# Kernel optimization log

Hardware: AMD Instinct MI355X
Metric: run time of the kernel (lower is better)

The kernel has to match this reference:

```python
import jax, jax.numpy as jnp
import numpy as np

INPUT_SIZE = 1024
HIDDEN_SIZE = 1024
BATCH = 8192


def setup_inputs() -> dict:
    key = jax.random.key(0)
    ks = jax.random.split(key, 10)
    H, I, B = HIDDEN_SIZE, INPUT_SIZE, BATCH
    s = 1.0 / np.sqrt(H)  # scale params so activations stay in sane range
    return {
        "input": jax.random.normal(ks[0], (B, I), jnp.float32),
        "hx": jax.random.normal(ks[1], (B, H), jnp.float32),
        "cx": jax.random.normal(ks[2], (B, H), jnp.float32),
        "att": jax.random.normal(ks[3], (B, I), jnp.float32),
        "weight_ih": jax.random.normal(ks[4], (4 * H, I), jnp.float32) * s,
        "weight_hh": jax.random.normal(ks[5], (4 * H, H), jnp.float32) * s,
        "bias_ih": jax.random.normal(ks[6], (4 * H,), jnp.float32),
        "bias_hh": jax.random.normal(ks[7], (4 * H,), jnp.float32),
        "weight_att": jax.random.normal(ks[8], (2 * H, I), jnp.float32) * s,
        "bias_att": jax.random.normal(ks[9], (2 * H,), jnp.float32),
    }


def reference(input, hx, cx, att, weight_ih, weight_hh, bias_ih, bias_hh,
              weight_att, bias_att):
    H = weight_hh.shape[1]
    # gates: [B, 4H]
    gates = input @ weight_ih.T + bias_ih + hx @ weight_hh.T + bias_hh
    att_gates = att @ weight_att.T + bias_att  # [B, 2H]
    ingate, forgetgate, cellgate, outgate = jnp.split(gates, 4, axis=1)
    ingate_att, attgate = jnp.split(att_gates, 2, axis=1)
    ingate = jax.nn.sigmoid(ingate)
    forgetgate = jax.nn.sigmoid(forgetgate)
    cellgate = jnp.tanh(cellgate)
    ingate_att = jax.nn.sigmoid(ingate_att)
    attgate = jnp.tanh(attgate)
    outgate = jax.nn.sigmoid(outgate)
    cy = forgetgate * cx + ingate * cellgate + ingate_att * attgate
    hy = outgate * jnp.tanh(cy)
    return (hy, cy)
```

## Files before the change

kernel.cpp:

```cpp
#include <hip/hip_runtime.h>


typedef __attribute__((ext_vector_type(8))) __bf16 bf16x8;
typedef __attribute__((ext_vector_type(8))) unsigned short ushort8;
typedef __attribute__((ext_vector_type(4))) float f32x4;

#define AS1 __attribute__((address_space(1)))
#define AS3 __attribute__((address_space(3)))

__device__ __forceinline__ void gld16(const unsigned short* g, unsigned short* l) {
    __builtin_amdgcn_global_load_lds((const AS1 void*)g, (AS3 void*)l, 16, 0, 0);
}

__device__ __forceinline__ unsigned short f2bf(float f) {
    unsigned int u = __builtin_bit_cast(unsigned int, f);
    u += 0x7fffu + ((u >> 16) & 1u);
    return (unsigned short)(u >> 16);
}

__device__ __forceinline__ float sigmoidf_(float x) { return 1.f / (1.f + __expf(-x)); }
__device__ __forceinline__ float tanhf_(float x) {
    float e = __expf(-2.f * fabsf(x));
    float t = (1.f - e) / (1.f + e);
    return x >= 0.f ? t : -t;
}

__device__ __forceinline__ bf16x8 ldfrag(const unsigned short* p) {
    return __builtin_bit_cast(bf16x8, *(const ushort8*)p);
}

#define BARRIER __builtin_amdgcn_s_barrier()
#define LGKM0   asm volatile("s_waitcnt lgkmcnt(0)" ::: "memory")
#define VMW_(n) asm volatile("s_waitcnt vmcnt(" #n ")" ::: "memory")
#define VMW(n)  VMW_(n)
#define PRIO1   __builtin_amdgcn_s_setprio(1)
#define PRIO0   __builtin_amdgcn_s_setprio(0)
#define MFMA16(a, b, c) __builtin_amdgcn_mfma_f32_16x16x32_bf16(a, b, c, 0, 0, 0)

__global__ void cast_all_k(const float* __restrict__ input, const float* __restrict__ hx,
                           const float* __restrict__ att,   const float* __restrict__ w_ih,
                           const float* __restrict__ w_hh,  const float* __restrict__ w_att,
                           const float* __restrict__ b_ih,  const float* __restrict__ b_hh,
                           unsigned short* __restrict__ XH, unsigned short* __restrict__ ATTb,
                           unsigned short* __restrict__ W4, unsigned short* __restrict__ WA,
                           float* __restrict__ bias4)
{
    int gid = blockIdx.x * blockDim.x + threadIdx.x;
    if (gid < 4096) bias4[gid] = b_ih[gid] + b_hh[gid];
    const int total = 4456448;
    for (int i = gid; i < total; i += gridDim.x * blockDim.x) {
        const float* src; unsigned short* dst; int ld, off, rel;
        if (i < 1048576)      { src = input; dst = XH;   ld = 2048; off = 0;    rel = i; }
        else if (i < 2097152) { src = hx;    dst = XH;   ld = 2048; off = 1024; rel = i - 1048576; }
        else if (i < 3145728) { src = att;   dst = ATTb; ld = 1024; off = 0;    rel = i - 2097152; }
        else if (i < 3670016) { src = w_ih;  dst = W4;   ld = 2048; off = 0;    rel = i - 3145728; }
        else if (i < 4194304) { src = w_hh;  dst = W4;   ld = 2048; off = 1024; rel = i - 3670016; }
        else                  { src = w_att; dst = WA;   ld = 1024; off = 0;    rel = i - 4194304; }
        int e = rel * 8;
        int r = e >> 10, c = e & 1023;
        const float4 v0 = *(const float4*)(src + e);
        const float4 v1 = *(const float4*)(src + e + 4);
        ushort8 p;
        p[0] = f2bf(v0.x); p[1] = f2bf(v0.y); p[2] = f2bf(v0.z); p[3] = f2bf(v0.w);
        p[4] = f2bf(v1.x); p[5] = f2bf(v1.y); p[6] = f2bf(v1.z); p[7] = f2bf(v1.w);
        *(ushort8*)(dst + r * ld + off + c) = p;
    }
}

__global__ __launch_bounds__(512, 2) void fused_gemm_k(
    const unsigned short* __restrict__ XH, const unsigned short* __restrict__ W4,
    const unsigned short* __restrict__ ATTb, const unsigned short* __restrict__ WA,
    const float* __restrict__ bias4, const float* __restrict__ bias_att,
    const float* __restrict__ cx, float* __restrict__ out)
{
    __shared__ unsigned short As[2][16384];
    __shared__ unsigned short Bs[2][16384];

    const int tid  = threadIdx.x;
    const int wave = tid >> 6, lane = tid & 63;
    const int l15 = lane & 15, quad = lane >> 4;
    const int wr = wave >> 2, wn = wave & 3;

    const int orig = blockIdx.x;
    const int k    = orig >> 3, xcd = orig & 7;
    const int row0 = (k >> 1) * 256;
    const int n0   = (xcd * 2 + (k & 1)) * 64;

    const int rl = tid >> 3;
    const int c8 = (tid & 7) ^ (rl & 7);
    unsigned aG = (unsigned)(row0 + rl) * 2048u + (unsigned)c8 * 8u;
    unsigned bG = (unsigned)(((rl >> 4) & 3) * 1024 + n0 + (rl & 15)) * 2048u + (unsigned)c8 * 8u;
    unsigned aA = (unsigned)(row0 + rl) * 1024u + (unsigned)c8 * 8u;
    unsigned bA = (unsigned)(((rl >> 4) & 1) * 1024 + n0 + ((rl >> 5) & 1) * 16 + (rl & 15)) * 1024u
                  + (unsigned)c8 * 8u;

    auto stageA_att = [&](int buf) {
#pragma unroll
        for (int h = 0; h < 2; ++h)
#pragma unroll
            for (int p = 0; p < 2; ++p)
                gld16(ATTb + aA + (unsigned)(h * 131072 + p * 65536),
                      &As[buf][h * 8192 + (tid + p * 512) * 8]);
        aA += 64;
    };
    auto stageB_att = [&](int buf) {
#pragma unroll
        for (int h = 0; h < 2; ++h)
            gld16(WA + bA + (unsigned)(h * 32768), &Bs[buf][(h * 512 + tid) * 8]);
        bA += 64;
    };
    auto stageA_g = [&](int buf) {
#pragma unroll
        for (int h = 0; h < 2; ++h)
#pragma unroll
            for (int p = 0; p < 2; ++p)
                gld16(XH + aG + (unsigned)(h * 262144 + p * 131072),
                      &As[buf][h * 8192 + (tid + p * 512) * 8]);
        aG += 64;
    };
    auto stageB_g = [&](int buf) {
#pragma unroll
        for (int h = 0; h < 2; ++h)
#pragma unroll
            for (int p = 0; p < 2; ++p)
                gld16(W4 + bG + (unsigned)(h * 65536 + p * 32768),
                      &Bs[buf][h * 8192 + (tid + p * 512) * 8]);
        bG += 64;
    };

    const int swz0 = (quad ^ (l15 & 7)) * 8;
    const int swz1 = ((4 + quad) ^ (l15 & 7)) * 8;
    const int aro  = (wr * 128 + l15) * 64;
    const int brG  = (wn * 64 + l15) * 64;
    const int brA  = (wn * 32 + l15) * 64;

    const f32x4 z = {0.f, 0.f, 0.f, 0.f};

    f32x4 acc2[8][2];
#pragma unroll
    for (int i = 0; i < 8; ++i) { acc2[i][0] = z; acc2[i][1] = z; }

    auto att_slice = [&](int buf, int sw) {
        bf16x8 aS[8], bS[2];
#pragma unroll
        for (int i = 0; i < 8; ++i) aS[i] = ldfrag(&As[buf][aro + i * 1024 + sw]);
#pragma unroll
        for (int j = 0; j < 2; ++j) bS[j] = ldfrag(&Bs[buf][brA + j * 1024 + sw]);
        BARRIER; LGKM0;
        PRIO1;
#pragma unroll
        for (int i = 0; i < 8; ++i)
#pragma unroll
            for (int j = 0; j < 2; ++j)
                acc2[i][j] = MFMA16(aS[i], bS[j], acc2[i][j]);
        PRIO0;
        BARRIER;
    };

    stageA_att(0); stageB_att(0);
    for (int g = 0; g < 8; ++g) {
        stageA_att(1); stageB_att(1);
        VMW(6); BARRIER;
        att_slice(0, swz0);
        att_slice(0, swz1);
        if (g < 7) { stageA_att(0); stageB_att(0); VMW(6); }
        else       { VMW(0); }
        BARRIER;
        att_slice(1, swz0);
        att_slice(1, swz1);
    }

    const int col = n0 + wn * 16 + l15;
    f32x4 attp[8];
    {
        const float ba0 = bias_att[col], ba1 = bias_att[1024 + col];
#pragma unroll
        for (int i = 0; i < 8; ++i)
#pragma unroll
            for (int r = 0; r < 4; ++r)
                attp[i][r] = sigmoidf_(acc2[i][0][r] + ba0) * tanhf_(acc2[i][1][r] + ba1);
    }

    f32x4 acc[8][4];
#pragma unroll
    for (int i = 0; i < 8; ++i)
#pragma unroll
        for (int j = 0; j < 4; ++j) acc[i][j] = z;

    auto gates_group = [&](int buf, bool iss) {
        bf16x8 aF[4], aH0[4], aH1[4], bS0[4], bS1[4];
#pragma unroll
        for (int i = 0; i < 4; ++i) aF[i] = ldfrag(&As[buf][aro + i * 1024 + swz0]);
#pragma unroll
        for (int j = 0; j < 4; ++j) bS0[j] = ldfrag(&Bs[buf][brG + j * 1024 + swz0]);
        BARRIER; LGKM0;
        PRIO1;
#pragma unroll
        for (int i = 0; i < 4; ++i)
#pragma unroll
            for (int j = 0; j < 4; ++j)
                acc[i][j] = MFMA16(aF[i], bS0[j], acc[i][j]);
        PRIO0;
        BARRIER;
#pragma unroll
        for (int i = 0; i < 4; ++i) aF[i] = ldfrag(&As[buf][aro + i * 1024 + swz1]);
#pragma unroll
        for (int j = 0; j < 4; ++j) bS1[j] = ldfrag(&Bs[buf][brG + j * 1024 + swz1]);
        BARRIER; LGKM0;
        PRIO1;
#pragma unroll
        for (int i = 0; i < 4; ++i)
#pragma unroll
            for (int j = 0; j < 4; ++j)
                acc[i][j] = MFMA16(aF[i], bS1[j], acc[i][j]);
        PRIO0;
        BARRIER;
#pragma unroll
        for (int i = 0; i < 4; ++i) {
            aH0[i] = ldfrag(&As[buf][aro + (4 + i) * 1024 + swz0]);
            aH1[i] = ldfrag(&As[buf][aro + (4 + i) * 1024 + swz1]);
        }
        if (iss) stageB_g(buf);
        BARRIER; LGKM0;
        PRIO1;
#pragma unroll
        for (int i = 0; i < 4; ++i)
#pragma unroll
            for (int j = 0; j < 4; ++j)
                acc[4 + i][j] = MFMA16(aH0[i], bS0[j], acc[4 + i][j]);
        PRIO0;
        BARRIER;
        if (iss) stageA_g(buf);
        PRIO1;
#pragma unroll
        for (int i = 0; i < 4; ++i)
#pragma unroll
            for (int j = 0; j < 4; ++j)
                acc[4 + i][j] = MFMA16(aH1[i], bS1[j], acc[4 + i][j]);
        PRIO0;
    };

    stageA_g(0); stageB_g(0); stageA_g(1); stageB_g(1);
    VMW(8); BARRIER;
#pragma unroll 2
    for (int t = 0; t < 30; ++t) {
        gates_group(t & 1, true);
        VMW(8); BARRIER;
    }
    gates_group(0, false); VMW(0); BARRIER;
    gates_group(1, false);

    float* sF = (float*)(&As[0][0]);
    float* sC = (float*)(&Bs[0][0]);
    const float bi  = bias4[col];
    const float bff = bias4[1024 + col];
    const float bg  = bias4[2048 + col];
    const float bo  = bias4[3072 + col];
    const int lcol  = wn * 16 + l15;
    const int CYOFF = 8192 * 1024;

#pragma unroll
    for (int i = 0; i < 8; ++i)
#pragma unroll
        for (int r = 0; r < 4; ++r) {
            const int lr = wr * 128 + i * 16 + quad * 4 + r;
            const int pc = lcol ^ (((lr >> 2) & 1) << 4);
            sF[lr * 64 + pc] = sigmoidf_(acc[i][1][r] + bff);
            sC[lr * 64 + pc] = sigmoidf_(acc[i][0][r] + bi) * tanhf_(acc[i][2][r] + bg)
                               + attp[i][r];
        }
    BARRIER;

    const int rr = tid >> 4;
    const int cc = (tid & 15) * 4;
#pragma unroll
    for (int p = 0; p < 8; ++p) {
        const int row = p * 32 + rr;
        const int pcc = cc ^ (((row >> 2) & 1) << 4);
        f32x4 fg4 = *(f32x4*)&sF[row * 64 + pcc];
        f32x4 cp4 = *(f32x4*)&sC[row * 64 + pcc];
        const float4 cx4 = *(const float4*)&cx[(row0 + row) * 1024 + n0 + cc];
        f32x4 cy4;
        cy4[0] = fg4[0] * cx4.x + cp4[0];
        cy4[1] = fg4[1] * cx4.y + cp4[1];
        cy4[2] = fg4[2] * cx4.z + cp4[2];
        cy4[3] = fg4[3] * cx4.w + cp4[3];
        *(f32x4*)&out[CYOFF + (row0 + row) * 1024 + n0 + cc] = cy4;
        *(f32x4*)&sF[row * 64 + pcc] = cy4;
    }
    BARRIER;

#pragma unroll
    for (int i = 0; i < 8; ++i)
#pragma unroll
        for (int r = 0; r < 4; ++r) {
            const int lr = wr * 128 + i * 16 + quad * 4 + r;
            const int pc = lcol ^ (((lr >> 2) & 1) << 4);
            sC[lr * 64 + pc] = sigmoidf_(acc[i][3][r] + bo);
        }
    BARRIER;

#pragma unroll
    for (int p = 0; p < 8; ++p) {
        const int row = p * 32 + rr;
        const int pcc = cc ^ (((row >> 2) & 1) << 4);
        f32x4 og4 = *(f32x4*)&sC[row * 64 + pcc];
        f32x4 cy4 = *(f32x4*)&sF[row * 64 + pcc];
        f32x4 hy4;
        hy4[0] = og4[0] * tanhf_(cy4[0]);
        hy4[1] = og4[1] * tanhf_(cy4[1]);
        hy4[2] = og4[2] * tanhf_(cy4[2]);
        hy4[3] = og4[3] * tanhf_(cy4[3]);
        *(f32x4*)&out[(row0 + row) * 1024 + n0 + cc] = hy4;
    }
}

extern "C" void kernel_launch(void* const* d_in, const int* in_sizes, int n_in,
                              void* d_out, int out_size, void* d_ws, size_t ws_size,
                              hipStream_t stream) {
    const float* input = (const float*)d_in[0];
    const float* hx    = (const float*)d_in[1];
    const float* cx    = (const float*)d_in[2];
    const float* att   = (const float*)d_in[3];
    const float* w_ih  = (const float*)d_in[4];
    const float* w_hh  = (const float*)d_in[5];
    const float* b_ih  = (const float*)d_in[6];
    const float* b_hh  = (const float*)d_in[7];
    const float* w_att = (const float*)d_in[8];
    const float* b_att = (const float*)d_in[9];
    float* out = (float*)d_out;

    char* ws = (char*)d_ws;
    unsigned short* XH   = (unsigned short*)(ws);
    unsigned short* ATTb = (unsigned short*)(ws + 33554432);
    unsigned short* W4   = (unsigned short*)(ws + 50331648);
    unsigned short* WA   = (unsigned short*)(ws + 67108864);
    float* bias4         = (float*)(ws + 71303168);

    cast_all_k<<<8704, 256, 0, stream>>>(input, hx, att, w_ih, w_hh, w_att,
                                         b_ih, b_hh, XH, ATTb, W4, WA, bias4);
    fused_gemm_k<<<512, 512, 0, stream>>>(XH, W4, ATTb, WA, bias4, b_att, cx, out);
}
```

Measured before the change: 403.4 us.

## Remap block-to-XCD tiling and reorder MFMA sub-tile schedule in gates loop

Changes the block index mapping so each XCD handles a contiguous set of row tiles across all column tiles, instead of a fixed set of column tiles. The intent is to improve L2 reuse of the activation rows within an XCD. The gates inner loop is also restructured to load both K-halves of the A fragments up front and to split B into low and high column pairs. This reorders the MFMA phases, interleaves LDS loads with compute differently, and raises register use for fragments. An extra barrier is added before the epilogue reuses shared memory.

```diff
diff --git a/kernel.cpp b/kernel.cpp
--- a/kernel.cpp
+++ b/kernel.cpp
@@ -81,10 +81,10 @@
     const int l15 = lane & 15, quad = lane >> 4;
     const int wr = wave >> 2, wn = wave & 3;
 
-    const int orig = blockIdx.x;
-    const int k    = orig >> 3, xcd = orig & 7;
-    const int row0 = (k >> 1) * 256;
-    const int n0   = (xcd * 2 + (k & 1)) * 64;
+    const int orig  = blockIdx.x;
+    const int xcd   = orig & 7, local = orig >> 3;
+    const int row0  = (xcd * 4 + (local & 3)) * 256;
+    const int n0    = (local >> 2) * 64;
 
     const int rl = tid >> 3;
     const int c8 = (tid & 7) ^ (rl & 7);
@@ -188,31 +188,42 @@
         for (int j = 0; j < 4; ++j) acc[i][j] = z;
 
     auto gates_group = [&](int buf, bool iss) {
-        bf16x8 aF[4], aH0[4], aH1[4], bS0[4], bS1[4];
-#pragma unroll
-        for (int i = 0; i < 4; ++i) aF[i] = ldfrag(&As[buf][aro + i * 1024 + swz0]);
-#pragma unroll
-        for (int j = 0; j < 4; ++j) bS0[j] = ldfrag(&Bs[buf][brG + j * 1024 + swz0]);
+        bf16x8 aF0[4], aF1[4], aH0[4], aH1[4], bL0[2], bL1[2], bH0[2], bH1[2];
+#pragma unroll
+        for (int i = 0; i < 4; ++i) {
+            aF0[i] = ldfrag(&As[buf][aro + i * 1024 + swz0]);
+            aF1[i] = ldfrag(&As[buf][aro + i * 1024 + swz1]);
+        }
+#pragma unroll
+        for (int j = 0; j < 2; ++j) {
+            bL0[j] = ldfrag(&Bs[buf][brG + j * 1024 + swz0]);
+            bL1[j] = ldfrag(&Bs[buf][brG + j * 1024 + swz1]);
+        }
         BARRIER; LGKM0;
         PRIO1;
 #pragma unroll
         for (int i = 0; i < 4; ++i)
 #pragma unroll
-            for (int j = 0; j < 4; ++j)
-                acc[i][j] = MFMA16(aF[i], bS0[j], acc[i][j]);
-        PRIO0;
-        BARRIER;
-#pragma unroll
-        for (int i = 0; i < 4; ++i) aF[i] = ldfrag(&As[buf][aro + i * 1024 + swz1]);
-#pragma unroll
-        for (int j = 0; j < 4; ++j) bS1[j] = ldfrag(&Bs[buf][brG + j * 1024 + swz1]);
+            for (int j = 0; j < 2; ++j) {
+                acc[i][j] = MFMA16(aF0[i], bL0[j], acc[i][j]);
+                acc[i][j] = MFMA16(aF1[i], bL1[j], acc[i][j]);
+            }
+        PRIO0;
+        BARRIER;
+#pragma unroll
+        for (int j = 0; j < 2; ++j) {
+            bH0[j] = ldfrag(&Bs[buf][brG + (2 + j) * 1024 + swz0]);
+            bH1[j] = ldfrag(&Bs[buf][brG + (2 + j) * 1024 + swz1]);
+        }
         BARRIER; LGKM0;
         PRIO1;
 #pragma unroll
         for (int i = 0; i < 4; ++i)
 #pragma unroll
-            for (int j = 0; j < 4; ++j)
-                acc[i][j] = MFMA16(aF[i], bS1[j], acc[i][j]);
+            for (int j = 0; j < 2; ++j) {
+                acc[i][2 + j] = MFMA16(aF0[i], bH0[j], acc[i][2 + j]);
+                acc[i][2 + j] = MFMA16(aF1[i], bH1[j], acc[i][2 + j]);
+            }
         PRIO0;
         BARRIER;
 #pragma unroll
@@ -226,8 +237,10 @@
 #pragma unroll
         for (int i = 0; i < 4; ++i)
 #pragma unroll
-            for (int j = 0; j < 4; ++j)
-                acc[4 + i][j] = MFMA16(aH0[i], bS0[j], acc[4 + i][j]);
+            for (int j = 0; j < 2; ++j) {
+                acc[4 + i][2 + j] = MFMA16(aH0[i], bH0[j], acc[4 + i][2 + j]);
+                acc[4 + i][2 + j] = MFMA16(aH1[i], bH1[j], acc[4 + i][2 + j]);
+            }
         PRIO0;
         BARRIER;
         if (iss) stageA_g(buf);
@@ -235,8 +248,10 @@
 #pragma unroll
         for (int i = 0; i < 4; ++i)
 #pragma unroll
-            for (int j = 0; j < 4; ++j)
-                acc[4 + i][j] = MFMA16(aH1[i], bS1[j], acc[4 + i][j]);
+            for (int j = 0; j < 2; ++j) {
+                acc[4 + i][j] = MFMA16(aH0[i], bL0[j], acc[4 + i][j]);
+                acc[4 + i][j] = MFMA16(aH1[i], bL1[j], acc[4 + i][j]);
+            }
         PRIO0;
     };
 
@@ -249,6 +264,7 @@
     }
     gates_group(0, false); VMW(0); BARRIER;
     gates_group(1, false);
+    BARRIER;
 
     float* sF = (float*)(&As[0][0]);
     float* sC = (float*)(&Bs[0][0]);
```

New measurement: 401.6 us. About the same (-0.4%).
